# Performance work log

Hardware: AMD Instinct MI355X
Metric: run time of the kernel (lower is better)

## Reference

```python
import jax, jax.numpy as jnp
import numpy as np

BST_DEPTH = 6
NB_SPLIT = 2**BST_DEPTH - 1          # 63 internal (split) nodes
NB_NODES = 2**(BST_DEPTH + 1) - 1    # 127 total nodes (heap layout)
SPLIT = np.arange(NB_SPLIT)
DESC_L = 2 * SPLIT + 1               # left children of split nodes
DESC_R = 2 * SPLIT + 2               # right children of split nodes


def setup_inputs() -> dict:
    key = jax.random.key(0)
    kx, ka = jax.random.split(key)
    x = jax.random.normal(kx, (131072, 512), dtype=jnp.float32)
    A = jax.random.uniform(ka, (NB_SPLIT, 512), dtype=jnp.float32)  # torch.rand init
    return {"x": x, "A": A}


def _compute_q(x, A):
    # XA[:, t] is the split score of internal node t; XA == XA[:, split_nodes]
    XA = x @ A.T                                         # [N, nb_split]
    q = jnp.ones((x.shape[0], NB_NODES), dtype=XA.dtype)  # [N, nb_nodes]
    # Seed children of each split node. NOTE: sequential semantics matter —
    # the right-child write reads q[:, SPLIT] AFTER the left-child write
    # (odd-indexed split nodes were just updated), matching torch in-place ops.
    q = q.at[:, DESC_L].set(jnp.minimum(q[:, SPLIT], XA))
    q = q.at[:, DESC_R].set(jnp.minimum(q[:, SPLIT], -XA))
    # Propagate the running min from parents down the tree, one sweep per level.
    for _ in range(BST_DEPTH):
        q = q.at[:, DESC_L].set(jnp.minimum(q[:, DESC_L], q[:, SPLIT]))
        q = q.at[:, DESC_R].set(jnp.minimum(q[:, DESC_R], q[:, SPLIT]))
    return q


def reference(x, A):
    q = _compute_q(x, A)
    z = jnp.clip(q, 0.0, 1.0)  # pruned=False: no QP pruning branch
    return z
```

## Files before the change

kernel.cpp:

```cpp
#include <hip/hip_runtime.h>
#include <cstdint>

#define KD 512
#define BM 256
#define BK 32
#define NSPLIT 63
#define NNODES 127
#define NTHREADS 512
#define LDX 40

typedef __attribute__((ext_vector_type(8))) short bf16x8;
typedef __attribute__((ext_vector_type(4))) float f32x4;

__device__ __forceinline__ unsigned short bf16_rtn(float f) {
    unsigned u = __builtin_bit_cast(unsigned int, f);
    u += 0x7FFFu + ((u >> 16) & 1u);
    return (unsigned short)(u >> 16);
}
__device__ __forceinline__ float bf16_f32(unsigned short h) {
    unsigned u = (unsigned)h << 16;
    return __builtin_bit_cast(float, u);
}

__global__ __launch_bounds__(NTHREADS, 2)
void lt_mfma_tree(const float* __restrict__ x, const float* __restrict__ A,
                  float* __restrict__ out) {
    __shared__ __align__(16) unsigned short sm[2 * BM * LDX + 2 * 64 * LDX];
    unsigned short* xh = sm;
    unsigned short* xl = sm + BM * LDX;
    unsigned short* bh = sm + 2 * BM * LDX;
    unsigned short* bl = bh + 64 * LDX;
    float* fl = reinterpret_cast<float*>(sm);

    const int tid = threadIdx.x;
    const int r0 = blockIdx.x * BM;

    const int srow = tid >> 1;
    const int skh  = (tid & 1) * 16;
    const int bn   = tid >> 3;
    const int bkq  = (tid & 7) * 4;

    float xr[16];
    float br[4] = {0.f, 0.f, 0.f, 0.f};

    {
        const float* px = &x[(size_t)(r0 + srow) * KD + skh];
#pragma unroll
        for (int p = 0; p < 4; ++p)
            *reinterpret_cast<float4*>(&xr[p * 4]) =
                *reinterpret_cast<const float4*>(&px[p * 4]);
        if (bn < NSPLIT)
            *reinterpret_cast<float4*>(br) =
                *reinterpret_cast<const float4*>(&A[(size_t)bn * KD + bkq]);
    }

    const int wave = tid >> 6;
    const int lane = tid & 63;
    const int m0   = wave * 32;
    const int fr   = lane & 15;
    const int kb   = (lane >> 4) * 8;

    f32x4 acc[2][4];
#pragma unroll
    for (int i = 0; i < 2; ++i)
#pragma unroll
        for (int j = 0; j < 4; ++j) acc[i][j] = (f32x4)(0.f);

    for (int kc = 0; kc < KD / BK; ++kc) {
        unsigned hw[8], lw[8];
#pragma unroll
        for (int i = 0; i < 8; ++i) {
            const unsigned short h0 = bf16_rtn(xr[2 * i]);
            const unsigned short h1 = bf16_rtn(xr[2 * i + 1]);
            const unsigned short l0 = bf16_rtn(xr[2 * i]     - bf16_f32(h0));
            const unsigned short l1 = bf16_rtn(xr[2 * i + 1] - bf16_f32(h1));
            hw[i] = (unsigned)h0 | ((unsigned)h1 << 16);
            lw[i] = (unsigned)l0 | ((unsigned)l1 << 16);
        }
        {
            int4 v;
            v.x = hw[0]; v.y = hw[1]; v.z = hw[2]; v.w = hw[3];
            *reinterpret_cast<int4*>(&xh[srow * LDX + skh]) = v;
            v.x = hw[4]; v.y = hw[5]; v.z = hw[6]; v.w = hw[7];
            *reinterpret_cast<int4*>(&xh[srow * LDX + skh + 8]) = v;
            v.x = lw[0]; v.y = lw[1]; v.z = lw[2]; v.w = lw[3];
            *reinterpret_cast<int4*>(&xl[srow * LDX + skh]) = v;
            v.x = lw[4]; v.y = lw[5]; v.z = lw[6]; v.w = lw[7];
            *reinterpret_cast<int4*>(&xl[srow * LDX + skh + 8]) = v;
        }
#pragma unroll
        for (int i = 0; i < 4; ++i) {
            const unsigned short h = bf16_rtn(br[i]);
            bh[bn * LDX + bkq + i] = h;
            bl[bn * LDX + bkq + i] = bf16_rtn(br[i] - bf16_f32(h));
        }
        __syncthreads();

        if (kc + 1 < KD / BK) {
            const float* px = &x[(size_t)(r0 + srow) * KD + (kc + 1) * BK + skh];
#pragma unroll
            for (int p = 0; p < 4; ++p)
                *reinterpret_cast<float4*>(&xr[p * 4]) =
                    *reinterpret_cast<const float4*>(&px[p * 4]);
            if (bn < NSPLIT)
                *reinterpret_cast<float4*>(br) =
                    *reinterpret_cast<const float4*>(&A[(size_t)bn * KD + (kc + 1) * BK + bkq]);
        }

        bf16x8 ah[2], al[2];
#pragma unroll
        for (int mf = 0; mf < 2; ++mf) {
            const int r = (m0 + mf * 16 + fr) * LDX + kb;
            ah[mf] = *reinterpret_cast<const bf16x8*>(&xh[r]);
            al[mf] = *reinterpret_cast<const bf16x8*>(&xl[r]);
        }
#pragma unroll
        for (int nf = 0; nf < 4; ++nf) {
            const int c = (nf * 16 + fr) * LDX + kb;
            const bf16x8 bhv = *reinterpret_cast<const bf16x8*>(&bh[c]);
            const bf16x8 blv = *reinterpret_cast<const bf16x8*>(&bl[c]);
#pragma unroll
            for (int mf = 0; mf < 2; ++mf) {
                acc[mf][nf] = __builtin_amdgcn_mfma_f32_16x16x32_bf16(ah[mf], bhv, acc[mf][nf], 0, 0, 0);
                acc[mf][nf] = __builtin_amdgcn_mfma_f32_16x16x32_bf16(ah[mf], blv, acc[mf][nf], 0, 0, 0);
                acc[mf][nf] = __builtin_amdgcn_mfma_f32_16x16x32_bf16(al[mf], bhv, acc[mf][nf], 0, 0, 0);
            }
        }
        __syncthreads();
    }

    const int drow = (lane >> 4) * 4;
    float* warea = fl + wave * 16 * 65;
    const int trow = lane >> 2;
    const int part = lane & 3;

#pragma unroll
    for (int ph = 0; ph < 2; ++ph) {
#pragma unroll
        for (int nf = 0; nf < 4; ++nf)
#pragma unroll
            for (int rg = 0; rg < 4; ++rg)
                warea[(drow + rg) * 65 + nf * 16 + fr] = acc[ph][nf][rg];
        __syncthreads();

        const float* srowp = warea + trow * 65;
        float* orow = out + (size_t)(r0 + m0 + ph * 16 + trow) * NNODES;
        float q[NNODES];
        q[0] = 1.f;
        if (part == 0) orow[0] = 1.f;
#pragma unroll
        for (int t = 0; t < NSPLIT; ++t) {
            const float s  = srowp[t];
            const float ql = fminf(q[t], s);
            const float qr = fminf(q[t], -s);
            q[2 * t + 1] = ql;
            q[2 * t + 2] = qr;
            const float zl = fminf(fmaxf(ql, 0.f), 1.f);
            const float zr = fminf(fmaxf(qr, 0.f), 1.f);
            if (((2 * t + 1) >> 5) == part) orow[2 * t + 1] = zl;
            if (((2 * t + 2) >> 5) == part) orow[2 * t + 2] = zr;
        }
        __syncthreads();
    }
}

extern "C" void kernel_launch(void* const* d_in, const int* in_sizes, int n_in,
                              void* d_out, int out_size, void* d_ws, size_t ws_size,
                              hipStream_t stream) {
    const float* x = (const float*)d_in[0];
    const float* A = (const float*)d_in[1];
    float* out = (float*)d_out;
    const int nrows = in_sizes[0] / KD;
    const int grid = nrows / BM;
    lt_mfma_tree<<<dim3(grid), dim3(NTHREADS), 0, stream>>>(x, A, out);
}
```

Measured before the change: 96.60 us.

## Load x fragments directly into registers and stage A in two halves

Each wave now reads its x rows straight from global memory into MFMA fragment registers, double-buffered one k-step ahead, and splits them into bf16 hi/lo in registers. This removes the x shared-memory staging and the two barriers per 32-wide k-step. The A matrix is split into hi/lo and written to LDS in two 256-wide halves, so the main loop needs only two barriers in total, and occupancy is raised to four blocks per CU. The cost is uncoalesced-ish per-lane 32-byte global reads of x and redundant hi/lo splitting work per wave. The MFMA issue order is also interleaved across the two row fragments.

```diff
diff --git a/kernel.cpp b/kernel.cpp
--- a/kernel.cpp
+++ b/kernel.cpp
@@ -1,64 +1,57 @@
 #include <hip/hip_runtime.h>
+#include <hip/hip_bf16.h>
 #include <cstdint>
 
 #define KD 512
 #define BM 256
-#define BK 32
+#define NT 512
+#define LDB 264
 #define NSPLIT 63
 #define NNODES 127
-#define NTHREADS 512
-#define LDX 40
 
 typedef __attribute__((ext_vector_type(8))) short bf16x8;
 typedef __attribute__((ext_vector_type(4))) float f32x4;
 
-__device__ __forceinline__ unsigned short bf16_rtn(float f) {
-    unsigned u = __builtin_bit_cast(unsigned int, f);
-    u += 0x7FFFu + ((u >> 16) & 1u);
-    return (unsigned short)(u >> 16);
+__device__ __forceinline__ unsigned short f2bf(float f) {
+    return __builtin_bit_cast(unsigned short, __float2bfloat16(f));
 }
-__device__ __forceinline__ float bf16_f32(unsigned short h) {
-    unsigned u = (unsigned)h << 16;
-    return __builtin_bit_cast(float, u);
+__device__ __forceinline__ float bf2f(unsigned short h) {
+    return __builtin_bit_cast(float, (unsigned)h << 16);
 }
 
-__global__ __launch_bounds__(NTHREADS, 2)
-void lt_mfma_tree(const float* __restrict__ x, const float* __restrict__ A,
-                  float* __restrict__ out) {
-    __shared__ __align__(16) unsigned short sm[2 * BM * LDX + 2 * 64 * LDX];
-    unsigned short* xh = sm;
-    unsigned short* xl = sm + BM * LDX;
-    unsigned short* bh = sm + 2 * BM * LDX;
-    unsigned short* bl = bh + 64 * LDX;
+__device__ __forceinline__ void split8(const float* __restrict__ f, bf16x8& h8, bf16x8& l8) {
+    union { bf16x8 v; unsigned short s[8]; } H, L;
+#pragma unroll
+    for (int i = 0; i < 8; ++i) {
+        const unsigned short hb = f2bf(f[i]);
+        H.s[i] = hb;
+        L.s[i] = f2bf(f[i] - bf2f(hb));
+    }
+    h8 = H.v; l8 = L.v;
+}
+
+__global__ __launch_bounds__(NT, 4)
+void lt_mfma2(const float* __restrict__ x, const float* __restrict__ A,
+              float* __restrict__ out) {
+    __shared__ __align__(16) unsigned short sm[2 * 64 * LDB];
+    unsigned short* bh = sm;
+    unsigned short* bl = sm + 64 * LDB;
     float* fl = reinterpret_cast<float*>(sm);
 
-    const int tid = threadIdx.x;
-    const int r0 = blockIdx.x * BM;
-
-    const int srow = tid >> 1;
-    const int skh  = (tid & 1) * 16;
-    const int bn   = tid >> 3;
-    const int bkq  = (tid & 7) * 4;
-
-    float xr[16];
-    float br[4] = {0.f, 0.f, 0.f, 0.f};
-
-    {
-        const float* px = &x[(size_t)(r0 + srow) * KD + skh];
-#pragma unroll
-        for (int p = 0; p < 4; ++p)
-            *reinterpret_cast<float4*>(&xr[p * 4]) =
-                *reinterpret_cast<const float4*>(&px[p * 4]);
-        if (bn < NSPLIT)
-            *reinterpret_cast<float4*>(br) =
-                *reinterpret_cast<const float4*>(&A[(size_t)bn * KD + bkq]);
-    }
-
+    const int tid  = threadIdx.x;
     const int wave = tid >> 6;
     const int lane = tid & 63;
-    const int m0   = wave * 32;
     const int fr   = lane & 15;
     const int kb   = (lane >> 4) * 8;
+    const int r0   = blockIdx.x * BM;
+    const int m0   = wave * 32;
+
+    const float* xr0p = x + (size_t)(r0 + m0 + fr) * KD + kb;
+    const float* xr1p = xr0p + 16 * KD;
+
+    const int brow = tid >> 3;
+    const int bkj  = (tid & 7) * 32;
+    const float* ap = A + (size_t)brow * KD + bkj;
 
     f32x4 acc[2][4];
 #pragma unroll
@@ -66,64 +59,71 @@
 #pragma unroll
         for (int j = 0; j < 4; ++j) acc[i][j] = (f32x4)(0.f);
 
-    for (int kc = 0; kc < KD / BK; ++kc) {
-        unsigned hw[8], lw[8];
+    float xb0[2][8], xb1[2][8];
 #pragma unroll
-        for (int i = 0; i < 8; ++i) {
-            const unsigned short h0 = bf16_rtn(xr[2 * i]);
-            const unsigned short h1 = bf16_rtn(xr[2 * i + 1]);
-            const unsigned short l0 = bf16_rtn(xr[2 * i]     - bf16_f32(h0));
-            const unsigned short l1 = bf16_rtn(xr[2 * i + 1] - bf16_f32(h1));
-            hw[i] = (unsigned)h0 | ((unsigned)h1 << 16);
-            lw[i] = (unsigned)l0 | ((unsigned)l1 << 16);
-        }
-        {
-            int4 v;
-            v.x = hw[0]; v.y = hw[1]; v.z = hw[2]; v.w = hw[3];
-            *reinterpret_cast<int4*>(&xh[srow * LDX + skh]) = v;
-            v.x = hw[4]; v.y = hw[5]; v.z = hw[6]; v.w = hw[7];
-            *reinterpret_cast<int4*>(&xh[srow * LDX + skh + 8]) = v;
-            v.x = lw[0]; v.y = lw[1]; v.z = lw[2]; v.w = lw[3];
-            *reinterpret_cast<int4*>(&xl[srow * LDX + skh]) = v;
-            v.x = lw[4]; v.y = lw[5]; v.z = lw[6]; v.w = lw[7];
-            *reinterpret_cast<int4*>(&xl[srow * LDX + skh + 8]) = v;
-        }
+    for (int p = 0; p < 2; ++p) {
+        *reinterpret_cast<float4*>(&xb0[0][p * 4]) =
+            *reinterpret_cast<const float4*>(xr0p + p * 4);
+        *reinterpret_cast<float4*>(&xb1[0][p * 4]) =
+            *reinterpret_cast<const float4*>(xr1p + p * 4);
+    }
+
 #pragma unroll
-        for (int i = 0; i < 4; ++i) {
-            const unsigned short h = bf16_rtn(br[i]);
-            bh[bn * LDX + bkq + i] = h;
-            bl[bn * LDX + bkq + i] = bf16_rtn(br[i] - bf16_f32(h));
+    for (int h = 0; h < 2; ++h) {
+#pragma unroll
+        for (int p8 = 0; p8 < 4; ++p8) {
+            float f[8];
+            if (brow < NSPLIT) {
+                *reinterpret_cast<float4*>(&f[0]) =
+                    *reinterpret_cast<const float4*>(ap + h * 256 + p8 * 8);
+                *reinterpret_cast<float4*>(&f[4]) =
+                    *reinterpret_cast<const float4*>(ap + h * 256 + p8 * 8 + 4);
+            } else {
+#pragma unroll
+                for (int i = 0; i < 8; ++i) f[i] = 0.f;
+            }
+            unsigned hw[4], lw[4];
+#pragma unroll
+            for (int i = 0; i < 4; ++i) {
+                const unsigned short h0 = f2bf(f[2 * i]);
+                const unsigned short h1 = f2bf(f[2 * i + 1]);
+                hw[i] = (unsigned)h0 | ((unsigned)h1 << 16);
+                lw[i] = (unsigned)f2bf(f[2 * i]     - bf2f(h0)) |
+                        ((unsigned)f2bf(f[2 * i + 1] - bf2f(h1)) << 16);
+            }
+            *reinterpret_cast<int4*>(&bh[brow * LDB + bkj + p8 * 8]) =
+                *reinterpret_cast<int4*>(hw);
+            *reinterpret_cast<int4*>(&bl[brow * LDB + bkj + p8 * 8]) =
+                *reinterpret_cast<int4*>(lw);
         }
         __syncthreads();
 
-        if (kc + 1 < KD / BK) {
-            const float* px = &x[(size_t)(r0 + srow) * KD + (kc + 1) * BK + skh];
 #pragma unroll
-            for (int p = 0; p < 4; ++p)
-                *reinterpret_cast<float4*>(&xr[p * 4]) =
-                    *reinterpret_cast<const float4*>(&px[p * 4]);
-            if (bn < NSPLIT)
-                *reinterpret_cast<float4*>(br) =
-                    *reinterpret_cast<const float4*>(&A[(size_t)bn * KD + (kc + 1) * BK + bkq]);
-        }
-
-        bf16x8 ah[2], al[2];
+        for (int t = 0; t < 8; ++t) {
+            const int gt = h * 8 + t;
+            if (gt + 1 < 16) {
 #pragma unroll
-        for (int mf = 0; mf < 2; ++mf) {
-            const int r = (m0 + mf * 16 + fr) * LDX + kb;
-            ah[mf] = *reinterpret_cast<const bf16x8*>(&xh[r]);
-            al[mf] = *reinterpret_cast<const bf16x8*>(&xl[r]);
-        }
+                for (int p = 0; p < 2; ++p) {
+                    *reinterpret_cast<float4*>(&xb0[(gt + 1) & 1][p * 4]) =
+                        *reinterpret_cast<const float4*>(xr0p + (gt + 1) * 32 + p * 4);
+                    *reinterpret_cast<float4*>(&xb1[(gt + 1) & 1][p * 4]) =
+                        *reinterpret_cast<const float4*>(xr1p + (gt + 1) * 32 + p * 4);
+                }
+            }
+            bf16x8 ah0, al0, ah1, al1;
+            split8(xb0[gt & 1], ah0, al0);
+            split8(xb1[gt & 1], ah1, al1);
 #pragma unroll
-        for (int nf = 0; nf < 4; ++nf) {
-            const int c = (nf * 16 + fr) * LDX + kb;
-            const bf16x8 bhv = *reinterpret_cast<const bf16x8*>(&bh[c]);
-            const bf16x8 blv = *reinterpret_cast<const bf16x8*>(&bl[c]);
-#pragma unroll
-            for (int mf = 0; mf < 2; ++mf) {
-                acc[mf][nf] = __builtin_amdgcn_mfma_f32_16x16x32_bf16(ah[mf], bhv, acc[mf][nf], 0, 0, 0);
-                acc[mf][nf] = __builtin_amdgcn_mfma_f32_16x16x32_bf16(ah[mf], blv, acc[mf][nf], 0, 0, 0);
-                acc[mf][nf] = __builtin_amdgcn_mfma_f32_16x16x32_bf16(al[mf], bhv, acc[mf][nf], 0, 0, 0);
+            for (int nf = 0; nf < 4; ++nf) {
+                const int off = (nf * 16 + fr) * LDB + t * 32 + kb;
+                const bf16x8 bhv = *reinterpret_cast<const bf16x8*>(&bh[off]);
+                const bf16x8 blv = *reinterpret_cast<const bf16x8*>(&bl[off]);
+                acc[0][nf] = __builtin_amdgcn_mfma_f32_16x16x32_bf16(ah0, bhv, acc[0][nf], 0, 0, 0);
+                acc[1][nf] = __builtin_amdgcn_mfma_f32_16x16x32_bf16(ah1, bhv, acc[1][nf], 0, 0, 0);
+                acc[0][nf] = __builtin_amdgcn_mfma_f32_16x16x32_bf16(al0, bhv, acc[0][nf], 0, 0, 0);
+                acc[1][nf] = __builtin_amdgcn_mfma_f32_16x16x32_bf16(al1, bhv, acc[1][nf], 0, 0, 0);
+                acc[0][nf] = __builtin_amdgcn_mfma_f32_16x16x32_bf16(ah0, blv, acc[0][nf], 0, 0, 0);
+                acc[1][nf] = __builtin_amdgcn_mfma_f32_16x16x32_bf16(ah1, blv, acc[1][nf], 0, 0, 0);
             }
         }
         __syncthreads();
@@ -172,5 +172,5 @@
     float* out = (float*)d_out;
     const int nrows = in_sizes[0] / KD;
     const int grid = nrows / BM;
-    lt_mfma_tree<<<dim3(grid), dim3(NTHREADS), 0, stream>>>(x, A, out);
+    lt_mfma2<<<dim3(grid), dim3(NT), 0, stream>>>(x, A, out);
 }
```

Measured after the change: 103.0 us. 1.07x slower.
